# Optimization experiments

Hardware: AMD Instinct MI355X
Metric: run time of the kernel (lower is better)

The kernel has to match this reference:

```python
import jax, jax.numpy as jnp
import numpy as np

D_MODEL = 1024
EXPAND = 2
D_INNER = EXPAND * D_MODEL          # 2048
HEADDIM = 64
NHEADS = D_INNER // HEADDIM         # 32
D_STATE = 128
NGROUPS = 1
D_CONV = 4
CONV_DIM = D_INNER + 2 * NGROUPS * D_STATE   # 2304
D_IN_PROJ = 2 * D_INNER + 2 * NGROUPS * D_STATE + NHEADS  # 4384
EPS = 1e-5


def setup_inputs() -> dict:
    key = jax.random.key(0)
    ks = jax.random.split(key, 12)
    x = jax.random.normal(ks[0], (2, 2048, D_MODEL), dtype=jnp.float32)
    in_proj_w = jax.random.normal(ks[1], (D_IN_PROJ, D_MODEL), dtype=jnp.float32) * 0.02
    conv_w = jax.random.normal(ks[2], (CONV_DIM, D_CONV), dtype=jnp.float32) * 0.2
    conv_b = jax.random.normal(ks[3], (CONV_DIM,), dtype=jnp.float32) * 0.02
    # dt_bias from inverse-softplus of dt ~ U(1e-3, 0.1)
    dt = jnp.exp(jax.random.uniform(ks[4], (NHEADS,)) * (np.log(0.1) - np.log(1e-3)) + np.log(1e-3))
    dt_bias = dt + jnp.log(-jnp.expm1(-dt))
    A_log = jnp.log(jax.random.uniform(ks[5], (NHEADS,), minval=1.0, maxval=16.0))
    D_skip = jnp.ones((NHEADS,), dtype=jnp.float32)
    norm_w = jnp.ones((D_INNER,), dtype=jnp.float32)
    out_w = jax.random.normal(ks[6], (D_MODEL, D_INNER), dtype=jnp.float32) * 0.02
    ln_g = jnp.ones((D_MODEL,), dtype=jnp.float32)
    ln_b = jnp.zeros((D_MODEL,), dtype=jnp.float32)
    return {"x": x, "in_proj_w": in_proj_w, "conv_w": conv_w, "conv_b": conv_b,
            "dt_bias": dt_bias, "A_log": A_log, "D_skip": D_skip, "norm_w": norm_w,
            "out_w": out_w, "ln_g": ln_g, "ln_b": ln_b}


def _depthwise_causal_conv(x, w, b):
    # x: (B, L, C); w: (C, K); causal depthwise conv (torch Conv1d groups=C, padding=K-1, truncated)
    K = w.shape[1]
    y = jax.lax.conv_general_dilated(
        x.transpose(0, 2, 1), w[:, None, :], (1,), [(K - 1, 0)],
        feature_group_count=w.shape[0], dimension_numbers=("NCH", "OIH", "NCH"))
    return y.transpose(0, 2, 1) + b


def _ssd_scan(xh, dt, A, Bm, Cm):
    # xh: (B,L,H,P), dt: (B,L,H), A: (H,), Bm/Cm: (B,L,N)  (ngroups=1)
    dA = jnp.exp(dt * A)  # (B,L,H)

    def step(h, inp):
        dA_t, dt_t, x_t, B_t, C_t = inp
        h = dA_t[..., None, None] * h + jnp.einsum("bh,bhp,bn->bhpn", dt_t, x_t, B_t)
        y = jnp.einsum("bhpn,bn->bhp", h, C_t)
        return h, y

    Bsz, L, H, P = xh.shape
    N = Bm.shape[-1]
    h0 = jnp.zeros((Bsz, H, P, N), dtype=xh.dtype)
    inputs = (dA.transpose(1, 0, 2), dt.transpose(1, 0, 2),
              xh.transpose(1, 0, 2, 3), Bm.transpose(1, 0, 2), Cm.transpose(1, 0, 2))
    _, ys = jax.lax.scan(step, h0, inputs)  # ys: (L,B,H,P)
    return ys.transpose(1, 0, 2, 3)


def reference(x, in_proj_w, conv_w, conv_b, dt_bias, A_log, D_skip, norm_w, out_w, ln_g, ln_b):
    B, L, D = x.shape
    residual = x  # D is a multiple of 8 -> pad branch is a no-op

    zxbcdt = jnp.einsum("bld,ed->ble", x, in_proj_w)  # (B,L,D_IN_PROJ)
    z = zxbcdt[..., :D_INNER]
    xBC = zxbcdt[..., D_INNER:D_INNER + CONV_DIM]
    dt = jax.nn.softplus(zxbcdt[..., D_INNER + CONV_DIM:] + dt_bias)  # (B,L,H)

    xBC = jax.nn.silu(_depthwise_causal_conv(xBC, conv_w, conv_b))
    xh = xBC[..., :D_INNER].reshape(B, L, NHEADS, HEADDIM)
    Bm = xBC[..., D_INNER:D_INNER + D_STATE]
    Cm = xBC[..., D_INNER + D_STATE:]

    A = -jnp.exp(A_log)  # (H,)
    y = _ssd_scan(xh, dt, A, Bm, Cm)          # (B,L,H,P)
    y = y + xh * D_skip[None, None, :, None]  # D skip connection
    y = y.reshape(B, L, D_INNER)

    # gated RMSNorm: normalize y * silu(z)
    y = y * jax.nn.silu(z)
    y = y * jax.lax.rsqrt(jnp.mean(y * y, axis=-1, keepdims=True) + EPS) * norm_w

    out = jnp.einsum("ble,de->bld", y, out_w)  # (B,L,D)

    # block LayerNorm + residual (dropout p=0 -> identity)
    mu = jnp.mean(out, axis=-1, keepdims=True)
    var = jnp.mean(jnp.square(out - mu), axis=-1, keepdims=True)
    out = (out - mu) * jax.lax.rsqrt(var + EPS) * ln_g + ln_b
    return out + residual
```

## Files before the change

### kernel.cpp

```cpp
#include <hip/hip_runtime.h>
#include <math.h>

#define D_MODEL   1024
#define D_INNER   2048
#define HEADDIM   64
#define NHEADS    32
#define D_STATE   128
#define D_CONV    4
#define CONV_DIM  2304
#define D_IN_PROJ 4384
#define NPAD      4480
#define LSEQ      2048
#define BATCH     2
#define NROWS     4096
#define NC        32

typedef __attribute__((ext_vector_type(8))) short short8_t;
typedef __attribute__((ext_vector_type(4))) float f32x4;

#define MFMA16(a, b, c) __builtin_amdgcn_mfma_f32_16x16x32_bf16(a, b, c, 0, 0, 0)

#define GLDS(g, l) __builtin_amdgcn_global_load_lds( \
    (const __attribute__((address_space(1))) unsigned int*)(g), \
    (__attribute__((address_space(3))) unsigned int*)(l), 16, 0, 0)

__device__ __forceinline__ unsigned short f2bf(float f) {
  union { float f; unsigned int u; } v; v.f = f;
  unsigned int u = v.u + 0x7FFFu + ((v.u >> 16) & 1u);
  return (unsigned short)(u >> 16);
}
__device__ __forceinline__ float bf2f(unsigned short h) {
  union { unsigned int u; float f; } v; v.u = ((unsigned int)h) << 16;
  return v.f;
}

__device__ __forceinline__ short8_t lds_frag(const unsigned short* base, int row,
                                             int col, int rowlen) {
  int off = (row * rowlen + col) * 2;
  off ^= (row & 7) << 4;
  return *reinterpret_cast<const short8_t*>(
      reinterpret_cast<const char*>(base) + off);
}
__device__ __forceinline__ void lds_w32(unsigned short* base, int row, int col,
                                        int rowlen, unsigned int val) {
  int off = (row * rowlen + col) * 2;
  off ^= (row & 7) << 4;
  *reinterpret_cast<unsigned int*>(reinterpret_cast<char*>(base) + off) = val;
}
__device__ __forceinline__ void lds_w16(unsigned short* base, int row, int col,
                                        int rowlen, unsigned short val) {
  int off = (row * rowlen + col) * 2;
  off ^= (row & 7) << 4;
  *reinterpret_cast<unsigned short*>(reinterpret_cast<char*>(base) + off) = val;
}
__device__ __forceinline__ unsigned short lds_r16(const unsigned short* base,
                                                  int row, int col, int rowlen) {
  int off = (row * rowlen + col) * 2;
  off ^= (row & 7) << 4;
  return *reinterpret_cast<const unsigned short*>(
      reinterpret_cast<const char*>(base) + off);
}

#define STAGE_TILE(bufA, bufB, kk0)                                        \
  do {                                                                     \
    _Pragma("unroll")                                                      \
    for (int i_ = 0; i_ < 4; ++i_) {                                       \
      int s_ = i_ * 256 + tid;                                             \
      int r_ = s_ >> 3;                                                    \
      int jc_ = ((s_ & 7) ^ (r_ & 7)) * 8;                                 \
      GLDS(&A[(size_t)(row0 + r_) * K + (kk0) + jc_], &(bufA)[s_ * 8]);    \
      GLDS(&B[(size_t)(col0 + r_) * K + (kk0) + jc_], &(bufB)[s_ * 8]);    \
    }                                                                      \
  } while (0)

template <int MODE>
__global__ __launch_bounds__(256) void gemm_db(
    const unsigned short* __restrict__ A, const unsigned short* __restrict__ B,
    void* __restrict__ Cout, float* __restrict__ dtraw, int N, int K) {
  extern __shared__ unsigned short lds[];
  const int tid = threadIdx.x;
  const int lin = blockIdx.y * gridDim.x + blockIdx.x;
  const int cpx = (gridDim.x * gridDim.y) >> 3;
  const int swz = (lin & 7) * cpx + (lin >> 3);
  const int row0 = (swz / gridDim.x) * 128;
  const int col0 = (swz % gridDim.x) * 128;

  const int l  = tid & 63;
  const int la = l & 15;
  const int lk = (l >> 4) * 8;
  const int w  = tid >> 6;
  const int wr = (w >> 1) * 64;
  const int wc = (w & 1) * 64;

  f32x4 acc[4][4];
  #pragma unroll
  for (int i = 0; i < 4; ++i)
    #pragma unroll
    for (int j = 0; j < 4; ++j) acc[i][j] = (f32x4){0.f, 0.f, 0.f, 0.f};

  const int NT = K >> 6;

  {
    unsigned short* dA = lds;
    unsigned short* dB = lds + 8192;
    STAGE_TILE(dA, dB, 0);
  }
  asm volatile("s_waitcnt vmcnt(0)" ::: "memory");
  __builtin_amdgcn_s_barrier();

  for (int t = 0; t < NT; ++t) {
    const int cur = t & 1;
    if (t + 1 < NT) {
      unsigned short* dA = lds + (cur ^ 1) * 16384;
      unsigned short* dB = dA + 8192;
      STAGE_TILE(dA, dB, (t + 1) << 6);
    }
    const unsigned short* aB = lds + cur * 16384;
    const unsigned short* bB = aB + 8192;
    #pragma unroll
    for (int kk = 0; kk < 2; ++kk) {
      short8_t af[4], bfr[4];
      #pragma unroll
      for (int mi = 0; mi < 4; ++mi)
        af[mi] = lds_frag(aB, wr + mi * 16 + la, kk * 32 + lk, 64);
      #pragma unroll
      for (int ni = 0; ni < 4; ++ni)
        bfr[ni] = lds_frag(bB, wc + ni * 16 + la, kk * 32 + lk, 64);
      #pragma unroll
      for (int mi = 0; mi < 4; ++mi)
        #pragma unroll
        for (int ni = 0; ni < 4; ++ni)
          acc[mi][ni] = MFMA16(af[mi], bfr[ni], acc[mi][ni]);
    }
    asm volatile("s_waitcnt vmcnt(0)" ::: "memory");
    __builtin_amdgcn_s_barrier();
  }

  #pragma unroll
  for (int mi = 0; mi < 4; ++mi)
    #pragma unroll
    for (int ni = 0; ni < 4; ++ni)
      #pragma unroll
      for (int r = 0; r < 4; ++r) {
        int gm = row0 + wr + mi * 16 + (l >> 4) * 4 + r;
        int gn = col0 + wc + ni * 16 + la;
        if (gn < N) {
          if constexpr (MODE == 0) {
            ((float*)Cout)[(size_t)gm * N + gn] = acc[mi][ni][r];
          } else {
            ((unsigned short*)Cout)[(size_t)gm * N + gn] = f2bf(acc[mi][ni][r]);
            if (gn >= N - 32)
              dtraw[(size_t)gm * 32 + (gn - (N - 32))] = acc[mi][ni][r];
          }
        }
      }
}

__device__ __forceinline__ short8_t cvt8(const float* s) {
  float4 a = *reinterpret_cast<const float4*>(s);
  float4 b = *reinterpret_cast<const float4*>(s + 4);
  short8_t o;
  o[0] = (short)f2bf(a.x); o[1] = (short)f2bf(a.y);
  o[2] = (short)f2bf(a.z); o[3] = (short)f2bf(a.w);
  o[4] = (short)f2bf(b.x); o[5] = (short)f2bf(b.y);
  o[6] = (short)f2bf(b.z); o[7] = (short)f2bf(b.w);
  return o;
}

__global__ __launch_bounds__(256) void cvt_all_kernel(
    const float* __restrict__ x, const float* __restrict__ w,
    const float* __restrict__ ow, unsigned short* __restrict__ xbf,
    unsigned short* __restrict__ wbf, unsigned short* __restrict__ owbf) {
  const long n1 = (long)NROWS * D_MODEL / 8;
  const long n2 = (long)NPAD * D_MODEL / 8;
  long i = (long)blockIdx.x * 256 + threadIdx.x;
  if (i < n1) {
    *reinterpret_cast<short8_t*>(&xbf[i * 8]) = cvt8(&x[i * 8]);
  } else if (i < n1 + n2) {
    long j = i - n1;
    int row = (int)(j >> 7);
    int c8  = (int)(j & 127) << 3;
    short8_t o = {0, 0, 0, 0, 0, 0, 0, 0};
    if (row < D_IN_PROJ) o = cvt8(&w[(size_t)row * D_MODEL + c8]);
    *reinterpret_cast<short8_t*>(&wbf[(size_t)row * D_MODEL + c8]) = o;
  } else {
    long j = i - n1 - n2;
    *reinterpret_cast<short8_t*>(&owbf[j * 8]) = cvt8(&ow[j * 8]);
  }
}

__global__ __launch_bounds__(256) void conv_silu_kernel(
    const unsigned short* __restrict__ zxb, const float* __restrict__ conv_w,
    const float* __restrict__ conv_b, unsigned short* __restrict__ xconv) {
  const int c  = blockIdx.x * 256 + threadIdx.x;
  const int l0 = blockIdx.y * 128;
  const int b  = blockIdx.z;
  const unsigned short* src = zxb + ((size_t)b * LSEQ) * D_IN_PROJ + D_INNER + c;
  const float w0 = conv_w[c * 4 + 0], w1 = conv_w[c * 4 + 1];
  const float w2 = conv_w[c * 4 + 2], w3 = conv_w[c * 4 + 3];
  const float bia = conv_b[c];
  float x0 = (l0 >= 3) ? bf2f(src[(size_t)(l0 - 3) * D_IN_PROJ]) : 0.f;
  float x1 = (l0 >= 2) ? bf2f(src[(size_t)(l0 - 2) * D_IN_PROJ]) : 0.f;
  float x2 = (l0 >= 1) ? bf2f(src[(size_t)(l0 - 1) * D_IN_PROJ]) : 0.f;
  unsigned short* dst = xconv + ((size_t)(b * LSEQ + l0)) * CONV_DIM + c;
  #pragma unroll 4
  for (int i = 0; i < 128; ++i) {
    float x3 = bf2f(src[(size_t)(l0 + i) * D_IN_PROJ]);
    float acc = fmaf(w3, x3, fmaf(w2, x2, fmaf(w1, x1, fmaf(w0, x0, bia))));
    float s = acc / (1.f + expf(-acc));
    dst[(size_t)i * CONV_DIM] = f2bf(s);
    x0 = x1; x1 = x2; x2 = x3;
  }
}

__global__ __launch_bounds__(256) void cumsum_kernel(
    const float* __restrict__ dtraw, const float* __restrict__ dt_bias,
    const float* __restrict__ A_log, float* __restrict__ dt_s,
    float* __restrict__ cumL) {
  int u = blockIdx.x * 4 + (threadIdx.x >> 6);
  int lane = threadIdx.x & 63;
  int h = u & 31;
  int bc = u >> 5;
  int row = bc * 64 + lane;
  float xr = dtraw[(size_t)row * 32 + h] + dt_bias[h];
  float dt = (xr > 20.f) ? xr : log1pf(expf(xr));
  dt_s[(size_t)row * NHEADS + h] = dt;
  float A = -expf(A_log[h]);
  float a = dt * A;
  #pragma unroll
  for (int off = 1; off < 64; off <<= 1) {
    float v = __shfl_up(a, off);
    if (lane >= off) a += v;
  }
  cumL[(size_t)u * 64 + lane] = a;
}

__global__ __launch_bounds__(256) void chunkstate_kernel(
    const unsigned short* __restrict__ xconv, const float* __restrict__ dt_s,
    const float* __restrict__ cumL, unsigned short* __restrict__ S) {
  const int bi = blockIdx.x;
  const int h  = bi & 31;
  const int bc = bi >> 5;
  const int row0 = bc * 64;
  const int tid = threadIdx.x;

  __shared__ unsigned short sBT[128 * 64];
  __shared__ unsigned short sXT[64 * 64];
  __shared__ float sw[64];

  if (tid < 64) {
    float L   = cumL[(size_t)bi * 64 + tid];
    float L63 = cumL[(size_t)bi * 64 + 63];
    sw[tid] = dt_s[(size_t)(row0 + tid) * NHEADS + h] * expf(L63 - L);
  }
  __syncthreads();

  #pragma unroll
  for (int i = 0; i < 16; ++i) {
    int idx = tid + i * 256;
    int s = idx >> 6, n2 = idx & 63;
    unsigned int v = *reinterpret_cast<const unsigned int*>(
        &xconv[(size_t)(row0 + s) * CONV_DIM + D_INNER + n2 * 2]);
    lds_w16(sBT, n2 * 2 + 0, s, 64, (unsigned short)v);
    lds_w16(sBT, n2 * 2 + 1, s, 64, (unsigned short)(v >> 16));
  }
  #pragma unroll
  for (int i = 0; i < 16; ++i) {
    int idx = tid + i * 256;
    int s = idx >> 6, p = idx & 63;
    float xv = bf2f(xconv[(size_t)(row0 + s) * CONV_DIM + h * HEADDIM + p]);
    lds_w16(sXT, p, s, 64, f2bf(xv * sw[s]));
  }
  __syncthreads();

  const int w  = tid >> 6;
  const int l  = tid & 63;
  const int la = l & 15;
  const int lk = (l >> 4) * 8;

  f32x4 acc[8];
  #pragma unroll
  for (int i = 0; i < 8; ++i) acc[i] = (f32x4){0.f, 0.f, 0.f, 0.f};

  #pragma unroll
  for (int ks = 0; ks < 2; ++ks) {
    short8_t a = lds_frag(sXT, 16 * w + la, ks * 32 + lk, 64);
    #pragma unroll
    for (int ni = 0; ni < 8; ++ni) {
      short8_t b = lds_frag(sBT, ni * 16 + la, ks * 32 + lk, 64);
      acc[ni] = MFMA16(a, b, acc[ni]);
    }
  }

  unsigned short* dst = S + (size_t)bi * (HEADDIM * D_STATE);
  #pragma unroll
  for (int ni = 0; ni < 8; ++ni)
    #pragma unroll
    for (int r = 0; r < 4; ++r) {
      int p = 16 * w + (l >> 4) * 4 + r;
      int n = ni * 16 + la;
      dst[p * D_STATE + n] = f2bf(acc[ni][r]);
    }
}

__global__ __launch_bounds__(256) void hscan_kernel(
    unsigned short* __restrict__ S, const float* __restrict__ cumL) {
  const int g  = blockIdx.x;
  const int bh = g >> 5;
  const int b  = bh >> 5;
  const int h  = bh & 31;
  const int e  = (g & 31) * 256 + threadIdx.x;

  float H = 0.f;
  #pragma unroll 4
  for (int c = 0; c < NC; ++c) {
    size_t u = (size_t)((b * NC + c) * NHEADS + h);
    float dA = expf(cumL[u * 64 + 63]);
    unsigned short sv = S[u * (HEADDIM * D_STATE) + e];
    S[u * (HEADDIM * D_STATE) + e] = f2bf(H);
    H = dA * H + bf2f(sv);
  }
}

__global__ __launch_bounds__(256) void chunk_kernel(
    const unsigned short* __restrict__ xconv, const float* __restrict__ dt_s,
    const float* __restrict__ cumL, const unsigned short* __restrict__ Hprev,
    const float* __restrict__ D_skip, unsigned short* __restrict__ y) {
  const int bi = blockIdx.x;
  const int h  = bi & 31;
  const int bc = bi >> 5;
  const int row0 = bc * 64;
  const int tid = threadIdx.x;

  __shared__ unsigned short sC[64 * 128];
  __shared__ unsigned short sB[64 * 128];
  __shared__ unsigned short sXT[64 * 64];
  __shared__ unsigned short sP[64 * 64];
  __shared__ float sL[64], sdt[64], seL[64];

  if (tid < 64) {
    float L = cumL[(size_t)bi * 64 + tid];
    sL[tid]  = L;
    seL[tid] = expf(L);
    sdt[tid] = dt_s[(size_t)(row0 + tid) * NHEADS + h];
  }

  #pragma unroll
  for (int i = 0; i < 8; ++i) {
    int idx = tid + i * 256;
    int r = idx >> 5, q = idx & 31;
    short8_t v = *reinterpret_cast<const short8_t*>(
        &xconv[(size_t)(row0 + r) * CONV_DIM + D_INNER + q * 8]);
    unsigned int u0 = (unsigned int)(unsigned short)v[0] |
                      ((unsigned int)(unsigned short)v[1] << 16);
    unsigned int u1 = (unsigned int)(unsigned short)v[2] |
                      ((unsigned int)(unsigned short)v[3] << 16);
    unsigned int u2 = (unsigned int)(unsigned short)v[4] |
                      ((unsigned int)(unsigned short)v[5] << 16);
    unsigned int u3 = (unsigned int)(unsigned short)v[6] |
                      ((unsigned int)(unsigned short)v[7] << 16);
    unsigned short* dstb = (q < 16) ? sB : sC;
    int cq = (q & 15) * 8;
    lds_w32(dstb, r, cq + 0, 128, u0);
    lds_w32(dstb, r, cq + 2, 128, u1);
    lds_w32(dstb, r, cq + 4, 128, u2);
    lds_w32(dstb, r, cq + 6, 128, u3);
  }
  #pragma unroll
  for (int i = 0; i < 16; ++i) {
    int idx = tid + i * 256;
    int s = idx >> 6, p = idx & 63;
    lds_w16(sXT, p, s, 64,
            xconv[(size_t)(row0 + s) * CONV_DIM + h * HEADDIM + p]);
  }
  __syncthreads();

  const int w  = tid >> 6;
  const int l  = tid & 63;
  const int la = l & 15;
  const int lk = (l >> 4) * 8;
  const int t0 = 16 * w;

  f32x4 g[4];
  #pragma unroll
  for (int i = 0; i < 4; ++i) g[i] = (f32x4){0.f, 0.f, 0.f, 0.f};
  #pragma unroll
  for (int ks = 0; ks < 4; ++ks) {
    short8_t a = lds_frag(sC, t0 + la, ks * 32 + lk, 128);
    #pragma unroll
    for (int si = 0; si < 4; ++si) {
      short8_t b = lds_frag(sB, si * 16 + la, ks * 32 + lk, 128);
      g[si] = MFMA16(a, b, g[si]);
    }
  }
  #pragma unroll
  for (int si = 0; si < 4; ++si)
    #pragma unroll
    for (int r = 0; r < 4; ++r) {
      int t = t0 + (l >> 4) * 4 + r;
      int s = si * 16 + la;
      float m = 0.f;
      if (s <= t) m = expf(sL[t] - sL[s]) * sdt[s] * g[si][r];
      lds_w16(sP, t, s, 64, f2bf(m));
    }
  __syncthreads();

  f32x4 o[4];
  #pragma unroll
  for (int i = 0; i < 4; ++i) o[i] = (f32x4){0.f, 0.f, 0.f, 0.f};

  const unsigned short* hb = Hprev + (size_t)bi * (HEADDIM * D_STATE);
  #pragma unroll
  for (int ks = 0; ks < 4; ++ks) {
    short8_t a = lds_frag(sC, t0 + la, ks * 32 + lk, 128);
    #pragma unroll
    for (int si = 0; si < 4; ++si) {
      int p = si * 16 + la;
      short8_t b = *reinterpret_cast<const short8_t*>(
          &hb[p * D_STATE + ks * 32 + lk]);
      o[si] = MFMA16(a, b, o[si]);
    }
  }
  #pragma unroll
  for (int si = 0; si < 4; ++si)
    #pragma unroll
    for (int r = 0; r < 4; ++r) {
      int t = t0 + (l >> 4) * 4 + r;
      o[si][r] *= seL[t];
    }
  #pragma unroll
  for (int ks = 0; ks < 2; ++ks) {
    short8_t a = lds_frag(sP, t0 + la, ks * 32 + lk, 64);
    #pragma unroll
    for (int si = 0; si < 4; ++si) {
      short8_t b = lds_frag(sXT, si * 16 + la, ks * 32 + lk, 64);
      o[si] = MFMA16(a, b, o[si]);
    }
  }
  const float Dh = D_skip[h];
  #pragma unroll
  for (int si = 0; si < 4; ++si)
    #pragma unroll
    for (int r = 0; r < 4; ++r) {
      int t = t0 + (l >> 4) * 4 + r;
      int p = si * 16 + la;
      float xv = bf2f(lds_r16(sXT, p, t, 64));
      y[(size_t)(row0 + t) * D_INNER + h * HEADDIM + p] = f2bf(o[si][r] + Dh * xv);
    }
}

__global__ __launch_bounds__(256) void gate_rms_kernel(
    unsigned short* __restrict__ y, const unsigned short* __restrict__ zxb,
    const float* __restrict__ norm_w) {
  const int row = blockIdx.x;
  const int tid = threadIdx.x;
  short8_t zv = *reinterpret_cast<const short8_t*>(
      &zxb[(size_t)row * D_IN_PROJ + tid * 8]);
  short8_t yv = *reinterpret_cast<short8_t*>(
      &y[(size_t)row * D_INNER + tid * 8]);
  float v[8];
  float acc = 0.f;
  #pragma unroll
  for (int i = 0; i < 8; ++i) {
    float z  = bf2f((unsigned short)zv[i]);
    float ys = bf2f((unsigned short)yv[i]);
    float gz = z / (1.f + expf(-z));
    float val = ys * gz;
    v[i] = val;
    acc = fmaf(val, val, acc);
  }
  #pragma unroll
  for (int off = 32; off; off >>= 1) acc += __shfl_xor(acc, off);
  __shared__ float wsum[4];
  if ((tid & 63) == 0) wsum[tid >> 6] = acc;
  __syncthreads();
  float total = wsum[0] + wsum[1] + wsum[2] + wsum[3];
  float scale = rsqrtf(total / (float)D_INNER + 1e-5f);
  short8_t o;
  #pragma unroll
  for (int i = 0; i < 8; ++i)
    o[i] = (short)f2bf(v[i] * scale * norm_w[tid * 8 + i]);
  *reinterpret_cast<short8_t*>(&y[(size_t)row * D_INNER + tid * 8]) = o;
}

__global__ __launch_bounds__(256) void ln_kernel(
    const float* __restrict__ o, const float* __restrict__ x,
    const float* __restrict__ lng, const float* __restrict__ lnb,
    float* __restrict__ out) {
  const int row = blockIdx.x;
  const int tid = threadIdx.x;
  float v[4];
  float s = 0.f, s2 = 0.f;
  #pragma unroll
  for (int i = 0; i < 4; ++i) {
    int d = i * 256 + tid;
    float t = o[(size_t)row * D_MODEL + d];
    v[i] = t;
    s += t;
    s2 = fmaf(t, t, s2);
  }
  #pragma unroll
  for (int off = 32; off; off >>= 1) {
    s  += __shfl_xor(s, off);
    s2 += __shfl_xor(s2, off);
  }
  __shared__ float sa[4], sb[4];
  if ((tid & 63) == 0) { sa[tid >> 6] = s; sb[tid >> 6] = s2; }
  __syncthreads();
  s  = sa[0] + sa[1] + sa[2] + sa[3];
  s2 = sb[0] + sb[1] + sb[2] + sb[3];
  float mu  = s / (float)D_MODEL;
  float var = s2 / (float)D_MODEL - mu * mu;
  float inv = rsqrtf(var + 1e-5f);
  #pragma unroll
  for (int i = 0; i < 4; ++i) {
    int d = i * 256 + tid;
    out[(size_t)row * D_MODEL + d] =
        (v[i] - mu) * inv * lng[d] + lnb[d] + x[(size_t)row * D_MODEL + d];
  }
}

extern "C" void kernel_launch(void* const* d_in, const int* in_sizes, int n_in,
                              void* d_out, int out_size, void* d_ws, size_t ws_size,
                              hipStream_t stream) {
  const float* x         = (const float*)d_in[0];
  const float* in_proj_w = (const float*)d_in[1];
  const float* conv_w    = (const float*)d_in[2];
  const float* conv_b    = (const float*)d_in[3];
  const float* dt_bias   = (const float*)d_in[4];
  const float* A_log     = (const float*)d_in[5];
  const float* D_skip    = (const float*)d_in[6];
  const float* norm_w    = (const float*)d_in[7];
  const float* out_w     = (const float*)d_in[8];
  const float* ln_g      = (const float*)d_in[9];
  const float* ln_b      = (const float*)d_in[10];
  float* out = (float*)d_out;

  char* ws = (char*)d_ws;
  unsigned short* zxb   = (unsigned short*)ws;
  float* outpre         = (float*)ws;
  char* p = ws + (size_t)NROWS * D_IN_PROJ * 2;
  float* dtraw = (float*)p;            p += (size_t)NROWS * 32 * 4;
  float* dt_s  = (float*)p;            p += (size_t)NROWS * 32 * 4;
  float* cumL  = (float*)p;            p += (size_t)BATCH * NC * NHEADS * 64 * 4;
  unsigned short* xconv = (unsigned short*)p;  p += (size_t)NROWS * CONV_DIM * 2;
  unsigned short* schp  = (unsigned short*)p;  p += (size_t)BATCH * NC * NHEADS * HEADDIM * D_STATE * 2;
  unsigned short* ybuf  = (unsigned short*)p;  p += (size_t)NROWS * D_INNER * 2;
  unsigned short* xbf   = (unsigned short*)p;  p += (size_t)NROWS * D_MODEL * 2;
  unsigned short* wbf   = (unsigned short*)p;  p += (size_t)NPAD * D_MODEL * 2;
  unsigned short* owbf  = (unsigned short*)p;

  (void)hipFuncSetAttribute(reinterpret_cast<const void*>(&gemm_db<1>),
                            hipFuncAttributeMaxDynamicSharedMemorySize, 65536);
  (void)hipFuncSetAttribute(reinterpret_cast<const void*>(&gemm_db<0>),
                            hipFuncAttributeMaxDynamicSharedMemorySize, 65536);

  {
    const long n1 = (long)NROWS * D_MODEL / 8;
    const long n2 = (long)NPAD * D_MODEL / 8;
    const long n3 = (long)D_MODEL * D_INNER / 8;
    int nblk = (int)((n1 + n2 + n3) / 256);
    cvt_all_kernel<<<dim3(nblk), dim3(256), 0, stream>>>(
        x, in_proj_w, out_w, xbf, wbf, owbf);
  }

  gemm_db<1><<<dim3(NPAD / 128, NROWS / 128), dim3(256), 65536, stream>>>(
      xbf, wbf, zxb, dtraw, D_IN_PROJ, D_MODEL);

  conv_silu_kernel<<<dim3(CONV_DIM / 256, LSEQ / 128, BATCH), dim3(256), 0, stream>>>(
      zxb, conv_w, conv_b, xconv);

  cumsum_kernel<<<dim3(BATCH * NC * NHEADS / 4), dim3(256), 0, stream>>>(
      dtraw, dt_bias, A_log, dt_s, cumL);

  chunkstate_kernel<<<dim3(BATCH * NC * NHEADS), dim3(256), 0, stream>>>(
      xconv, dt_s, cumL, schp);

  hscan_kernel<<<dim3(BATCH * NHEADS * 32), dim3(256), 0, stream>>>(
      schp, cumL);

  chunk_kernel<<<dim3(BATCH * NC * NHEADS), dim3(256), 0, stream>>>(
      xconv, dt_s, cumL, schp, D_skip, ybuf);

  gate_rms_kernel<<<dim3(NROWS), dim3(256), 0, stream>>>(
      ybuf, zxb, norm_w);

  gemm_db<0><<<dim3(D_MODEL / 128, NROWS / 128), dim3(256), 65536, stream>>>(
      ybuf, owbf, outpre, nullptr, D_MODEL, D_INNER);

  ln_kernel<<<dim3(NROWS), dim3(256), 0, stream>>>(
      outpre, x, ln_g, ln_b, out);
}
```

Baseline: 298.8 us.

## Prefetch two GEMM tiles ahead and vectorize conv and state-scan kernels

The GEMM now issues loads for the first two K-tiles up front. Each iteration waits with a partial vmcnt so the next tile's loads stay in flight, and the freed buffer is refilled two steps ahead after the compute. MFMA issue is wrapped in raised wave priority. The conv+SiLU and inter-chunk state scan kernels are changed from one scalar bf16 element per thread to 8-wide vector loads and stores, which cuts instruction count and improves coalescing. The vectorized hscan launches far fewer threads, and the conv kernel uses shorter strips, so parallelism and occupancy change.

```diff
diff --git a/kernel.cpp b/kernel.cpp
--- a/kernel.cpp
+++ b/kernel.cpp
@@ -101,20 +101,22 @@
   const int NT = K >> 6;
 
   {
-    unsigned short* dA = lds;
-    unsigned short* dB = lds + 8192;
-    STAGE_TILE(dA, dB, 0);
-  }
-  asm volatile("s_waitcnt vmcnt(0)" ::: "memory");
-  __builtin_amdgcn_s_barrier();
+    unsigned short* dA0 = lds;
+    unsigned short* dB0 = lds + 8192;
+    STAGE_TILE(dA0, dB0, 0);
+    unsigned short* dA1 = lds + 16384;
+    unsigned short* dB1 = dA1 + 8192;
+    STAGE_TILE(dA1, dB1, 64);
+  }
 
   for (int t = 0; t < NT; ++t) {
     const int cur = t & 1;
-    if (t + 1 < NT) {
-      unsigned short* dA = lds + (cur ^ 1) * 16384;
-      unsigned short* dB = dA + 8192;
-      STAGE_TILE(dA, dB, (t + 1) << 6);
-    }
+    if (t + 1 < NT)
+      asm volatile("s_waitcnt vmcnt(8)" ::: "memory");
+    else
+      asm volatile("s_waitcnt vmcnt(0)" ::: "memory");
+    __builtin_amdgcn_s_barrier();
+
     const unsigned short* aB = lds + cur * 16384;
     const unsigned short* bB = aB + 8192;
     #pragma unroll
@@ -126,14 +128,20 @@
       #pragma unroll
       for (int ni = 0; ni < 4; ++ni)
         bfr[ni] = lds_frag(bB, wc + ni * 16 + la, kk * 32 + lk, 64);
+      __builtin_amdgcn_s_setprio(1);
       #pragma unroll
       for (int mi = 0; mi < 4; ++mi)
         #pragma unroll
         for (int ni = 0; ni < 4; ++ni)
           acc[mi][ni] = MFMA16(af[mi], bfr[ni], acc[mi][ni]);
-    }
-    asm volatile("s_waitcnt vmcnt(0)" ::: "memory");
+      __builtin_amdgcn_s_setprio(0);
+    }
     __builtin_amdgcn_s_barrier();
+    if (t + 2 < NT) {
+      unsigned short* dA = lds + cur * 16384;
+      unsigned short* dB = dA + 8192;
+      STAGE_TILE(dA, dB, (t + 2) << 6);
+    }
   }
 
   #pragma unroll
@@ -189,27 +197,64 @@
   }
 }
 
+#define NCG (CONV_DIM / 8)
+
 __global__ __launch_bounds__(256) void conv_silu_kernel(
     const unsigned short* __restrict__ zxb, const float* __restrict__ conv_w,
     const float* __restrict__ conv_b, unsigned short* __restrict__ xconv) {
-  const int c  = blockIdx.x * 256 + threadIdx.x;
-  const int l0 = blockIdx.y * 128;
-  const int b  = blockIdx.z;
-  const unsigned short* src = zxb + ((size_t)b * LSEQ) * D_IN_PROJ + D_INNER + c;
-  const float w0 = conv_w[c * 4 + 0], w1 = conv_w[c * 4 + 1];
-  const float w2 = conv_w[c * 4 + 2], w3 = conv_w[c * 4 + 3];
-  const float bia = conv_b[c];
-  float x0 = (l0 >= 3) ? bf2f(src[(size_t)(l0 - 3) * D_IN_PROJ]) : 0.f;
-  float x1 = (l0 >= 2) ? bf2f(src[(size_t)(l0 - 2) * D_IN_PROJ]) : 0.f;
-  float x2 = (l0 >= 1) ? bf2f(src[(size_t)(l0 - 1) * D_IN_PROJ]) : 0.f;
-  unsigned short* dst = xconv + ((size_t)(b * LSEQ + l0)) * CONV_DIM + c;
-  #pragma unroll 4
-  for (int i = 0; i < 128; ++i) {
-    float x3 = bf2f(src[(size_t)(l0 + i) * D_IN_PROJ]);
-    float acc = fmaf(w3, x3, fmaf(w2, x2, fmaf(w1, x1, fmaf(w0, x0, bia))));
-    float s = acc / (1.f + expf(-acc));
-    dst[(size_t)i * CONV_DIM] = f2bf(s);
-    x0 = x1; x1 = x2; x2 = x3;
+  int v = blockIdx.x * 256 + threadIdx.x;
+  int cg = v % NCG;
+  int rest = v / NCG;
+  int strip = rest & 31;
+  int b = rest >> 5;
+  const int c0 = cg * 8;
+  const int l0 = strip * 64;
+
+  float4 wv[8];
+  float bi[8];
+  #pragma unroll
+  for (int j = 0; j < 8; ++j) {
+    wv[j] = *reinterpret_cast<const float4*>(&conv_w[(c0 + j) * 4]);
+    bi[j] = conv_b[c0 + j];
+  }
+
+  const unsigned short* src =
+      zxb + ((size_t)b * LSEQ) * D_IN_PROJ + D_INNER + c0;
+  unsigned short* dst =
+      xconv + ((size_t)(b * LSEQ + l0)) * CONV_DIM + c0;
+
+  float h0[8] = {}, h1[8] = {}, h2[8] = {};
+  if (l0 >= 3) {
+    short8_t a = *reinterpret_cast<const short8_t*>(
+        &src[(size_t)(l0 - 3) * D_IN_PROJ]);
+    short8_t bq = *reinterpret_cast<const short8_t*>(
+        &src[(size_t)(l0 - 2) * D_IN_PROJ]);
+    short8_t c = *reinterpret_cast<const short8_t*>(
+        &src[(size_t)(l0 - 1) * D_IN_PROJ]);
+    #pragma unroll
+    for (int j = 0; j < 8; ++j) {
+      h0[j] = bf2f((unsigned short)a[j]);
+      h1[j] = bf2f((unsigned short)bq[j]);
+      h2[j] = bf2f((unsigned short)c[j]);
+    }
+  }
+
+  for (int i = 0; i < 64; ++i) {
+    short8_t xv = *reinterpret_cast<const short8_t*>(
+        &src[(size_t)(l0 + i) * D_IN_PROJ]);
+    short8_t ov;
+    #pragma unroll
+    for (int j = 0; j < 8; ++j) {
+      float x3 = bf2f((unsigned short)xv[j]);
+      float acc = fmaf(wv[j].w, x3,
+                  fmaf(wv[j].z, h2[j],
+                  fmaf(wv[j].y, h1[j],
+                  fmaf(wv[j].x, h0[j], bi[j]))));
+      float s = acc / (1.f + expf(-acc));
+      ov[j] = (short)f2bf(s);
+      h0[j] = h1[j]; h1[j] = h2[j]; h2[j] = x3;
+    }
+    *reinterpret_cast<short8_t*>(&dst[(size_t)i * CONV_DIM]) = ov;
   }
 }
 
@@ -305,20 +350,24 @@
 
 __global__ __launch_bounds__(256) void hscan_kernel(
     unsigned short* __restrict__ S, const float* __restrict__ cumL) {
-  const int g  = blockIdx.x;
-  const int bh = g >> 5;
-  const int b  = bh >> 5;
-  const int h  = bh & 31;
-  const int e  = (g & 31) * 256 + threadIdx.x;
-
-  float H = 0.f;
-  #pragma unroll 4
+  int v = blockIdx.x * 256 + threadIdx.x;
+  int e8 = (v & 1023) * 8;
+  int bh = v >> 10;
+  int b = bh >> 5, h = bh & 31;
+
+  float H[8] = {};
   for (int c = 0; c < NC; ++c) {
     size_t u = (size_t)((b * NC + c) * NHEADS + h);
     float dA = expf(cumL[u * 64 + 63]);
-    unsigned short sv = S[u * (HEADDIM * D_STATE) + e];
-    S[u * (HEADDIM * D_STATE) + e] = f2bf(H);
-    H = dA * H + bf2f(sv);
+    unsigned short* sp = S + u * (HEADDIM * D_STATE) + e8;
+    short8_t sv = *reinterpret_cast<const short8_t*>(sp);
+    short8_t ov;
+    #pragma unroll
+    for (int j = 0; j < 8; ++j) {
+      ov[j] = (short)f2bf(H[j]);
+      H[j] = fmaf(dA, H[j], bf2f((unsigned short)sv[j]));
+    }
+    *reinterpret_cast<short8_t*>(sp) = ov;
   }
 }
 
@@ -567,7 +616,7 @@
   gemm_db<1><<<dim3(NPAD / 128, NROWS / 128), dim3(256), 65536, stream>>>(
       xbf, wbf, zxb, dtraw, D_IN_PROJ, D_MODEL);
 
-  conv_silu_kernel<<<dim3(CONV_DIM / 256, LSEQ / 128, BATCH), dim3(256), 0, stream>>>(
+  conv_silu_kernel<<<dim3(NCG * 32 * BATCH / 256), dim3(256), 0, stream>>>(
       zxb, conv_w, conv_b, xconv);
 
   cumsum_kernel<<<dim3(BATCH * NC * NHEADS / 4), dim3(256), 0, stream>>>(
@@ -576,7 +625,7 @@
   chunkstate_kernel<<<dim3(BATCH * NC * NHEADS), dim3(256), 0, stream>>>(
       xconv, dt_s, cumL, schp);
 
-  hscan_kernel<<<dim3(BATCH * NHEADS * 32), dim3(256), 0, stream>>>(
+  hscan_kernel<<<dim3(BATCH * NHEADS * 1024 / 256), dim3(256), 0, stream>>>(
       schp, cumL);
 
   chunk_kernel<<<dim3(BATCH * NC * NHEADS), dim3(256), 0, stream>>>(
```

Measured after the change: 321.3 us. +7.5%, slower.
